# Kernel optimization log

Hardware: AMD Instinct MI355X
Metric: run time of the kernel (lower is better)

## Reference

```python
import jax, jax.numpy as jnp
import numpy as np

B, T, W, L, H = 32, 1024, 512, 12, 8
CH = W // H                      # per-head dim = 64
IN_CH = 3 + 6 + T                # x + params + class embedding channels = 1033
DFF = 4 * W
NEG = -100000.0
SCALE = 1.0 / np.sqrt(np.sqrt(CH))


def _layernorm(x, g, b, eps=1e-5):
    m = jnp.mean(x, axis=-1, keepdims=True)
    v = jnp.mean(jnp.square(x - m), axis=-1, keepdims=True)
    return (x - m) * jax.lax.rsqrt(v + eps) * g + b


def setup_inputs() -> dict:
    key = jax.random.key(0)
    ks = jax.random.split(key, 40)
    std = 0.25 * np.sqrt(1.0 / W)  # init_scale used inside Transformer

    def n(k, shape, s=std):
        return (jax.random.normal(k, shape, jnp.float32) * s).astype(jnp.float32)

    inp = {
        'x': jax.random.normal(ks[0], (B, 3, T), jnp.float32),
        'params': jax.random.normal(ks[1], (B, 6, T), jnp.float32),
        'mask': (jax.random.uniform(ks[2], (B, T)) > 0.2).astype(jnp.float32),
        'class_emb': jax.random.normal(ks[3], (T, T), jnp.float32),  # nn.Embedding(n_ctx, n_ctx)
        'w_in': n(ks[4], (IN_CH, W), 0.02), 'b_in': jnp.zeros((W,), jnp.float32),
        'ln_pre_g': jnp.ones((W,), jnp.float32), 'ln_pre_b': jnp.zeros((W,), jnp.float32),
        'qkv_w': n(ks[5], (L, W, 3 * W)), 'qkv_b': jnp.zeros((L, 3 * W), jnp.float32),
        'attn_pw': n(ks[6], (L, W, W)), 'attn_pb': jnp.zeros((L, W), jnp.float32),
        'ln1_g': jnp.ones((L, W), jnp.float32), 'ln1_b': jnp.zeros((L, W), jnp.float32),
        'fc_w': n(ks[7], (L, W, DFF)), 'fc_b': jnp.zeros((L, DFF), jnp.float32),
        'fcp_w': n(ks[8], (L, DFF, W)), 'fcp_b': jnp.zeros((L, W), jnp.float32),
        'ln2_g': jnp.ones((L, W), jnp.float32), 'ln2_b': jnp.zeros((L, W), jnp.float32),
        'ln_post_g': jnp.ones((W,), jnp.float32), 'ln_post_b': jnp.zeros((W,), jnp.float32),
        'w_out': n(ks[9], (W, W), 0.02), 'b_out': jnp.zeros((W,), jnp.float32),
        'agg_fc_w': n(ks[10], (W, DFF)), 'agg_fc_b': jnp.zeros((DFF,), jnp.float32),
        'agg_pw': n(ks[11], (DFF, W)), 'agg_pb': jnp.zeros((W,), jnp.float32),
    }
    return inp


def _block(h, p):
    qw, qb, pw, pb, l1g, l1b, fw, fb, gw, gb, l2g, l2b = p
    hn = _layernorm(h, l1g, l1b)
    qkv = (hn @ qw + qb).reshape(B, T, H, 3 * CH)
    q, k, v = jnp.split(qkv, 3, axis=-1)
    att = jnp.einsum('bthc,bshc->bhts', q * SCALE, k * SCALE)
    att = jax.nn.softmax(att.astype(jnp.float32), axis=-1)  # softmax in fp32
    o = jnp.einsum('bhts,bshc->bthc', att, v).reshape(B, T, W)
    h = h + o @ pw + pb
    hn2 = _layernorm(h, l2g, l2b)
    h = h + jax.nn.gelu(hn2 @ fw + fb, approximate=False) @ gw + gb
    return h, None


def reference(x, params, mask, class_emb, w_in, b_in, ln_pre_g, ln_pre_b,
              qkv_w, qkv_b, attn_pw, attn_pb, ln1_g, ln1_b, fc_w, fc_b,
              fcp_w, fcp_b, ln2_g, ln2_b, ln_post_g, ln_post_b, w_out, b_out,
              agg_fc_w, agg_fc_b, agg_pw, agg_pb):
    # concatenate params and class-embedding channels: [B, 1033, T]
    ce = jnp.broadcast_to(class_emb.T[None], (B, T, T))  # class_embed.transpose(1,2)
    xin = jnp.concatenate([x, params, ce], axis=1)
    h = jnp.einsum('bct,cw->btw', xin, w_in) + b_in      # input_proj on [B,T,1033]
    h = _layernorm(h, ln_pre_g, ln_pre_b)
    h, _ = jax.lax.scan(_block, h,
                        (qkv_w, qkv_b, attn_pw, attn_pb, ln1_g, ln1_b,
                         fc_w, fc_b, fcp_w, fcp_b, ln2_g, ln2_b))
    h = _layernorm(h, ln_post_g, ln_post_b)
    h = (h @ w_out + b_out).transpose(0, 2, 1)           # [B, 512, T]
    h = h * mask[:, None, :]
    pooled = jnp.max(h + (1.0 - mask[:, None, :]) * NEG, axis=2)  # [B, 512]
    z = jax.nn.gelu(pooled @ agg_fc_w + agg_fc_b, approximate=False) @ agg_pw + agg_pb
    return (z, h)
```

## Files before the change

kernel.cpp:

```cpp
#include <hip/hip_runtime.h>
#include <hip/hip_bf16.h>


typedef unsigned short u16;
typedef unsigned int u32;
typedef __attribute__((ext_vector_type(8))) short bf16x8;
typedef __attribute__((ext_vector_type(8))) unsigned short us8;
typedef __attribute__((ext_vector_type(4))) unsigned short us4;
typedef __attribute__((ext_vector_type(4))) float f32x4;

__device__ __forceinline__ float bf2f(u16 s) {
  union { u32 u; float f; } c; c.u = ((u32)s) << 16; return c.f;
}
__device__ __forceinline__ u16 f2bf(float f) {
  __hip_bfloat16 h = __float2bfloat16(f);
  union { __hip_bfloat16 h; u16 u; } c; c.h = h; return c.u;
}
__device__ __forceinline__ float gelu_f(float v) {
  return 0.5f * v * (1.0f + erff(v * 0.7071067811865475f));
}
__device__ __forceinline__ void gl2lds16(const u16* g, u16* l) {
  __builtin_amdgcn_global_load_lds((const __attribute__((address_space(1))) void*)g,
                                   (__attribute__((address_space(3))) void*)l, 16, 0, 0);
}
__device__ __forceinline__ f32x4 mfma16(bf16x8 a, bf16x8 b, f32x4 c) {
  return __builtin_amdgcn_mfma_f32_16x16x32_bf16(a, b, c, 0, 0, 0);
}
__device__ __forceinline__ int swz(int row) { return (row ^ (row >> 3)) & 7; }

template <int EPI>
__global__ __launch_bounds__(512)
void gemm_bt(const u16* __restrict__ A, const u16* __restrict__ Bt,
             const float* __restrict__ bias, float* __restrict__ Cf,
             u16* __restrict__ Cb, u16* __restrict__ Vt, int K, int lda, int ldb, int ldc)
{
  __shared__ __align__(16) u16 As[2][256 * 32];
  __shared__ __align__(16) u16 Bs[2][128 * 32];
  const int tid = threadIdx.x;
  const int lane = tid & 63, wid = tid >> 6;
  const int wm = wid & 3, wn = wid >> 2;
  const int nbx = gridDim.x;
  const int nwg = nbx * gridDim.y;
  int lin = blockIdx.y * nbx + blockIdx.x;
  lin = (lin & 7) * (nwg >> 3) + (lin >> 3);
  const long m0 = (long)(lin / nbx) * 256, n0 = (long)(lin % nbx) * 128;

  const int c0 = tid, c1 = tid + 512;
  const int kc0 = (c0 & 3) ^ (((c0 >> 2) >> 1) & 3);
  const int kc1 = (c1 & 3) ^ (((c1 >> 2) >> 1) & 3);
  const int kcb = (tid & 3) ^ (((tid >> 2) >> 1) & 3);
  const u16* aS0 = A + (m0 + (c0 >> 2)) * (long)lda + kc0 * 8;
  const u16* aS1 = A + (m0 + (c1 >> 2)) * (long)lda + kc1 * 8;
  const u16* bS0 = Bt + (n0 + (tid >> 2)) * (long)ldb + kcb * 8;

  f32x4 acc[4][4] = {};
  const int cl4 = lane & 15;
  const int gph = ((lane >> 4) ^ ((cl4 >> 1) & 3)) * 8;
  const int aro = (wm * 64 + cl4) * 32 + gph;
  const int bro = (wn * 64 + cl4) * 32 + gph;
  const int nt = K >> 5;

#define STAGE_AB(buf, k0_)                          \
  gl2lds16(aS0 + (k0_), As[buf] + c0 * 8);          \
  gl2lds16(aS1 + (k0_), As[buf] + c1 * 8);          \
  gl2lds16(bS0 + (k0_), Bs[buf] + tid * 8);

  STAGE_AB(0, 0);
  for (int t = 0; t < nt; ++t) {
    const int cur = t & 1;
    if (t < nt - 1) {
      STAGE_AB(cur ^ 1, (t + 1) * 32);
      asm volatile("s_waitcnt vmcnt(3)" ::: "memory");
    } else {
      asm volatile("s_waitcnt vmcnt(0)" ::: "memory");
    }
    __builtin_amdgcn_s_barrier();
    bf16x8 af[4], bfr[4];
#pragma unroll
    for (int i = 0; i < 4; ++i) af[i] = *(const bf16x8*)(As[cur] + aro + i * 16 * 32);
#pragma unroll
    for (int j = 0; j < 4; ++j) bfr[j] = *(const bf16x8*)(Bs[cur] + bro + j * 16 * 32);
    __builtin_amdgcn_s_setprio(1);
#pragma unroll
    for (int i = 0; i < 4; ++i)
#pragma unroll
      for (int j = 0; j < 4; ++j)
        acc[i][j] = mfma16(af[i], bfr[j], acc[i][j]);
    __builtin_amdgcn_s_setprio(0);
    __builtin_amdgcn_s_barrier();
  }
#undef STAGE_AB
  const int rg = (lane >> 4) * 4, cl = lane & 15;
#pragma unroll
  for (int i = 0; i < 4; ++i) {
#pragma unroll
    for (int j = 0; j < 4; ++j) {
      const long row = m0 + wm * 64 + i * 16 + rg;
      const long col = n0 + wn * 64 + j * 16 + cl;
      const float bv = bias ? bias[col] : 0.0f;
      if (EPI == 4) {
        const int hh = (int)col / 192, off = (int)col - hh * 192;
        if (off < 128) {
#pragma unroll
          for (int r = 0; r < 4; ++r)
            Cb[(row + r) * ldc + col] = f2bf(acc[i][j][r] + bv);
        } else {
          us4 pk;
#pragma unroll
          for (int r = 0; r < 4; ++r) pk[r] = f2bf(acc[i][j][r] + bv);
          const long bl = row >> 10, t0 = row & 1023;
          *(us4*)(Vt + (((bl * 8 + hh) * 64 + (off - 128)) << 10) + t0) = pk;
        }
      } else {
#pragma unroll
        for (int r = 0; r < 4; ++r) {
          float v = acc[i][j][r] + bv;
          long idx = (row + r) * ldc + col;
          if (EPI == 0) Cf[idx] = v;
          else if (EPI == 1) Cb[idx] = f2bf(v);
          else if (EPI == 2) Cf[idx] += v;
          else Cb[idx] = f2bf(gelu_f(v));
        }
      }
    }
  }
}

__global__ __launch_bounds__(512)
void attn_k(const u16* __restrict__ qkv, const u16* __restrict__ vt, u16* __restrict__ o)
{
  __shared__ __align__(16) u16 Qs[128 * 64];
  __shared__ __align__(16) u16 Ks[2][64 * 64];
  __shared__ __align__(16) u16 Vts[2][64 * 64];
  const int tid = threadIdx.x, lane = tid & 63, wid = tid >> 6;
  int lin = blockIdx.x;
  lin = (lin & 7) * 128 + (lin >> 3);
  const int qt = lin & 7, hh = (lin >> 3) & 7, b = lin >> 6;
  const long rowbase = (long)b * 1024;
  const long vbase = (((long)b * 8 + hh) * 64) * 1024;
  const int g = lane >> 4, cl = lane & 15;
  u16* Psw = Qs + wid * 1024;

#pragma unroll
  for (int it = 0; it < 2; ++it) {
    int c = tid + it * 512;
    int row = c >> 3, c8s = (c & 7) ^ swz(row);
    gl2lds16(qkv + (rowbase + qt * 128 + row) * 1536 + hh * 192 + c8s * 8, Qs + c * 8);
  }
#define STAGE_KV(buf, kt_)                                                            \
  {                                                                                   \
    int row = tid >> 3, c8s = (tid & 7) ^ swz(row);                                   \
    gl2lds16(qkv + (rowbase + (kt_) * 64 + row) * 1536 + hh * 192 + 64 + c8s * 8,     \
             Ks[buf] + tid * 8);                                                      \
    gl2lds16(vt + vbase + (long)row * 1024 + (kt_) * 64 + c8s * 8, Vts[buf] + tid * 8); \
  }
  STAGE_KV(0, 0);

  float m = -3.0e38f, l = 0.f;
  f32x4 oacc[4] = {};
  const int Rq = wid * 16 + cl, sq = swz(Rq) << 3;
  const int spw = swz(cl) << 3;
  bf16x8 aq[2];

  for (int kt = 0; kt < 16; ++kt) {
    const int cur = kt & 1;
    if (kt < 15) {
      STAGE_KV(cur ^ 1, kt + 1);
      asm volatile("s_waitcnt vmcnt(2)" ::: "memory");
    } else {
      asm volatile("s_waitcnt vmcnt(0)" ::: "memory");
    }
    __builtin_amdgcn_s_barrier();
    if (kt == 0) {
#pragma unroll
      for (int kb = 0; kb < 2; ++kb)
        aq[kb] = *(const bf16x8*)(Qs + Rq * 64 + ((kb * 32 + g * 8) ^ sq));
    }
    f32x4 s[4] = {};
    __builtin_amdgcn_s_setprio(1);
#pragma unroll
    for (int j = 0; j < 4; ++j) {
      const int Rk = j * 16 + cl, sk = swz(Rk) << 3;
#pragma unroll
      for (int kb = 0; kb < 2; ++kb) {
        bf16x8 bk = *(const bf16x8*)(Ks[cur] + Rk * 64 + ((kb * 32 + g * 8) ^ sk));
        s[j] = mfma16(bk, aq[kb], s[j]);
      }
    }
    __builtin_amdgcn_s_setprio(0);
    float mx = s[0][0];
#pragma unroll
    for (int j = 0; j < 4; ++j)
#pragma unroll
      for (int r = 0; r < 4; ++r) mx = fmaxf(mx, s[j][r]);
    mx *= 0.125f;
    mx = fmaxf(mx, __shfl_xor(mx, 16, 64));
    mx = fmaxf(mx, __shfl_xor(mx, 32, 64));
    if (!__all(mx <= m + 8.f)) {
      const float mnew = fmaxf(m, mx);
      const float al = __expf(m - mnew);
      m = mnew;
      l *= al;
      float alr[4];
#pragma unroll
      for (int r = 0; r < 4; ++r) alr[r] = __shfl(al, (lane & 48) | (g * 4 + r), 64);
#pragma unroll
      for (int cb = 0; cb < 4; ++cb) {
        f32x4 t = oacc[cb];
        t[0] *= alr[0]; t[1] *= alr[1]; t[2] *= alr[2]; t[3] *= alr[3];
        oacc[cb] = t;
      }
    }
    float p[4][4], ts = 0.f;
#pragma unroll
    for (int j = 0; j < 4; ++j)
#pragma unroll
      for (int r = 0; r < 4; ++r) {
        p[j][r] = __expf(s[j][r] * 0.125f - m);
        ts += p[j][r];
      }
    ts += __shfl_xor(ts, 16, 64);
    ts += __shfl_xor(ts, 32, 64);
    l += ts;
#pragma unroll
    for (int j = 0; j < 4; ++j) {
      us4 pk;
      pk[0] = f2bf(p[j][0]); pk[1] = f2bf(p[j][1]);
      pk[2] = f2bf(p[j][2]); pk[3] = f2bf(p[j][3]);
      *(us4*)(&Psw[cl * 64 + ((j * 16 + g * 4) ^ spw)]) = pk;
    }
    asm volatile("s_waitcnt lgkmcnt(0)" ::: "memory");
    bf16x8 pa[2];
#pragma unroll
    for (int kb = 0; kb < 2; ++kb)
      pa[kb] = *(const bf16x8*)(&Psw[cl * 64 + ((kb * 32 + g * 8) ^ spw)]);
    __builtin_amdgcn_s_setprio(1);
#pragma unroll
    for (int kb = 0; kb < 2; ++kb)
#pragma unroll
      for (int cb = 0; cb < 4; ++cb) {
        const int ch = cb * 16 + cl;
        bf16x8 vb = *(const bf16x8*)(Vts[cur] + ch * 64 + ((kb * 32 + g * 8) ^ (swz(ch) << 3)));
        oacc[cb] = mfma16(pa[kb], vb, oacc[cb]);
      }
    __builtin_amdgcn_s_setprio(0);
    __builtin_amdgcn_s_barrier();
  }
#undef STAGE_KV
  float lr[4];
#pragma unroll
  for (int r = 0; r < 4; ++r) lr[r] = __shfl(l, (lane & 48) | (g * 4 + r), 64);
#pragma unroll
  for (int cb = 0; cb < 4; ++cb)
#pragma unroll
    for (int r = 0; r < 4; ++r) {
      long row = rowbase + qt * 128 + wid * 16 + g * 4 + r;
      o[row * 512 + hh * 64 + cb * 16 + cl] = f2bf(oacc[cb][r] / lr[r]);
    }
}

template <int MODE>
__global__ __launch_bounds__(256)
void ln_k(const float* __restrict__ in_, const float* __restrict__ gg,
          const float* __restrict__ bb, void* __restrict__ out_)
{
  const long row = (long)blockIdx.x * 4 + (threadIdx.x >> 6);
  const int lane = threadIdx.x & 63;
  float x[8];
  const float* p = in_ + row * 512 + lane * 8;
  *(float4*)(x) = *(const float4*)(p);
  *(float4*)(x + 4) = *(const float4*)(p + 4);
  float s = 0.f;
#pragma unroll
  for (int j = 0; j < 8; ++j) s += x[j];
#pragma unroll
  for (int off = 1; off < 64; off <<= 1) s += __shfl_xor(s, off, 64);
  const float mean = s * (1.0f / 512.0f);
  float vs = 0.f;
#pragma unroll
  for (int j = 0; j < 8; ++j) { float d = x[j] - mean; vs += d * d; }
#pragma unroll
  for (int off = 1; off < 64; off <<= 1) vs += __shfl_xor(vs, off, 64);
  const float rstd = rsqrtf(vs * (1.0f / 512.0f) + 1e-5f);
  if (MODE == 0) {
    float y[8];
#pragma unroll
    for (int j = 0; j < 8; ++j)
      y[j] = (x[j] - mean) * rstd * gg[lane * 8 + j] + bb[lane * 8 + j];
    float* q = (float*)out_ + row * 512 + lane * 8;
    *(float4*)(q) = *(const float4*)(y);
    *(float4*)(q + 4) = *(const float4*)(y + 4);
  } else {
    us8 ov;
#pragma unroll
    for (int j = 0; j < 8; ++j)
      ov[j] = f2bf((x[j] - mean) * rstd * gg[lane * 8 + j] + bb[lane * 8 + j]);
    *(us8*)((u16*)out_ + row * 512 + lane * 8) = ov;
  }
}

__global__ __launch_bounds__(256)
void embed_k(const float* __restrict__ x, const float* __restrict__ par,
             const float* __restrict__ E, const float* __restrict__ w_in,
             const float* __restrict__ b_in, float* __restrict__ h)
{
  const long bt = blockIdx.x;
  const int b = (int)(bt >> 10), t = (int)(bt & 1023);
  float xs[9];
#pragma unroll
  for (int c = 0; c < 3; ++c) xs[c] = x[((long)b * 3 + c) * 1024 + t];
#pragma unroll
  for (int c = 0; c < 6; ++c) xs[3 + c] = par[((long)b * 6 + c) * 1024 + t];
  for (int w = threadIdx.x; w < 512; w += 256) {
    float a = E[(long)t * 512 + w] + b_in[w];
#pragma unroll
    for (int c = 0; c < 9; ++c) a += xs[c] * w_in[c * 512 + w];
    h[bt * 512 + w] = a;
  }
}

__global__ __launch_bounds__(256)
void tr_k(const float* __restrict__ in, u16* __restrict__ out, int R, int C)
{
  __shared__ u16 tile[32][33];
  const int r0 = blockIdx.y * 32, c0 = blockIdx.x * 32;
  const int tx = threadIdx.x & 31, ty = threadIdx.x >> 5;
  for (int rr = ty; rr < 32; rr += 8) tile[rr][tx] = f2bf(in[(long)(r0 + rr) * C + c0 + tx]);
  __syncthreads();
  for (int rr = ty; rr < 32; rr += 8) out[(long)(c0 + rr) * R + r0 + tx] = tile[tx][rr];
}

__global__ __launch_bounds__(256)
void cast_k(const float* __restrict__ in, u16* __restrict__ out, long n)
{
  long i = ((long)blockIdx.x * 256 + threadIdx.x) * 4;
  if (i + 3 < n) {
    float4 v = *(const float4*)(in + i);
    out[i] = f2bf(v.x); out[i + 1] = f2bf(v.y); out[i + 2] = f2bf(v.z); out[i + 3] = f2bf(v.w);
  }
}

__global__ __launch_bounds__(256)
void pool1_k(const float* __restrict__ hm, const float* __restrict__ mask, float* __restrict__ part)
{
  const int c = blockIdx.x, b = blockIdx.y;
  const int t0 = c * 128;
  const int w0 = threadIdx.x, w1 = threadIdx.x + 256;
  float m0 = -3.0e38f, m1 = -3.0e38f;
  for (int t = 0; t < 128; ++t) {
    const float mv = mask[b * 1024 + t0 + t];
    const float neg = (1.0f - mv) * (-100000.0f);
    const float* row = hm + ((long)b * 1024 + t0 + t) * 512;
    m0 = fmaxf(m0, row[w0] * mv + neg);
    m1 = fmaxf(m1, row[w1] * mv + neg);
  }
  part[((long)b * 8 + c) * 512 + w0] = m0;
  part[((long)b * 8 + c) * 512 + w1] = m1;
}
__global__ __launch_bounds__(256)
void pool2_k(const float* __restrict__ part, float* __restrict__ pooled)
{
  const int b = blockIdx.y;
  const int w = blockIdx.x * 256 + threadIdx.x;
  float m = -3.0e38f;
#pragma unroll
  for (int c = 0; c < 8; ++c) m = fmaxf(m, part[((long)b * 8 + c) * 512 + w]);
  pooled[b * 512 + w] = m;
}

__global__ __launch_bounds__(256)
void tout_k(const float* __restrict__ hm, const float* __restrict__ mask, float* __restrict__ outh)
{
  __shared__ float tile[64][65];
  const int t0 = blockIdx.x * 64, w0 = blockIdx.y * 64, b = blockIdx.z;
  const int tx = threadIdx.x & 63, ty = threadIdx.x >> 6;
  for (int i = ty; i < 64; i += 4)
    tile[i][tx] = hm[((long)b * 1024 + t0 + i) * 512 + w0 + tx];
  __syncthreads();
  const float mv = mask[b * 1024 + t0 + tx];
  for (int i = ty; i < 64; i += 4)
    outh[((long)b * 512 + w0 + i) * 1024 + t0 + tx] = tile[tx][i] * mv;
}

__global__ __launch_bounds__(256)
void agg1p_k(const float* __restrict__ pooled, const float* __restrict__ wf,
             float* __restrict__ part)
{
  const int b = blockIdx.z, kc = blockIdx.y;
  const int n = blockIdx.x * 256 + threadIdx.x;
  float acc = 0.f;
  const int k0 = kc * 64;
#pragma unroll 8
  for (int k = 0; k < 64; ++k) acc += pooled[b * 512 + k0 + k] * wf[(long)(k0 + k) * 2048 + n];
  part[((long)b * 8 + kc) * 2048 + n] = acc;
}
__global__ __launch_bounds__(256)
void agg1c_k(const float* __restrict__ part, const float* __restrict__ bf_,
             float* __restrict__ z1)
{
  const int b = blockIdx.y;
  const int n = blockIdx.x * 256 + threadIdx.x;
  float acc = 0.f;
#pragma unroll
  for (int c = 0; c < 8; ++c) acc += part[((long)b * 8 + c) * 2048 + n];
  z1[(long)b * 2048 + n] = gelu_f(acc + bf_[n]);
}
__global__ __launch_bounds__(256)
void agg2p_k(const float* __restrict__ z1, const float* __restrict__ wp,
             float* __restrict__ part)
{
  const int b = blockIdx.z, kc = blockIdx.y;
  const int n = blockIdx.x * 256 + threadIdx.x;
  float acc = 0.f;
  const int k0 = kc * 256;
#pragma unroll 8
  for (int k = 0; k < 256; ++k) acc += z1[(long)b * 2048 + k0 + k] * wp[(long)(k0 + k) * 512 + n];
  part[((long)b * 8 + kc) * 512 + n] = acc;
}
__global__ __launch_bounds__(256)
void agg2c_k(const float* __restrict__ part, const float* __restrict__ bp,
             float* __restrict__ zo)
{
  const int b = blockIdx.y;
  const int n = blockIdx.x * 256 + threadIdx.x;
  float acc = 0.f;
#pragma unroll
  for (int c = 0; c < 8; ++c) acc += part[((long)b * 8 + c) * 512 + n];
  zo[b * 512 + n] = acc + bp[n];
}

extern "C" void kernel_launch(void* const* d_in, const int* in_sizes, int n_in,
                              void* d_out, int out_size, void* d_ws, size_t ws_size,
                              hipStream_t stream)
{
  (void)in_sizes; (void)n_in; (void)out_size; (void)ws_size;
  const float* x        = (const float*)d_in[0];
  const float* params   = (const float*)d_in[1];
  const float* mask     = (const float*)d_in[2];
  const float* class_emb= (const float*)d_in[3];
  const float* w_in     = (const float*)d_in[4];
  const float* b_in     = (const float*)d_in[5];
  const float* ln_pre_g = (const float*)d_in[6];
  const float* ln_pre_b = (const float*)d_in[7];
  const float* qkv_w    = (const float*)d_in[8];
  const float* qkv_b    = (const float*)d_in[9];
  const float* attn_pw  = (const float*)d_in[10];
  const float* attn_pb  = (const float*)d_in[11];
  const float* ln1_g    = (const float*)d_in[12];
  const float* ln1_b    = (const float*)d_in[13];
  const float* fc_w     = (const float*)d_in[14];
  const float* fc_b     = (const float*)d_in[15];
  const float* fcp_w    = (const float*)d_in[16];
  const float* fcp_b    = (const float*)d_in[17];
  const float* ln2_g    = (const float*)d_in[18];
  const float* ln2_b    = (const float*)d_in[19];
  const float* ln_post_g= (const float*)d_in[20];
  const float* ln_post_b= (const float*)d_in[21];
  const float* w_out    = (const float*)d_in[22];
  const float* b_out    = (const float*)d_in[23];
  const float* agg_fc_w = (const float*)d_in[24];
  const float* agg_fc_b = (const float*)d_in[25];
  const float* agg_pw   = (const float*)d_in[26];
  const float* agg_pb   = (const float*)d_in[27];

  float* out_f = (float*)d_out;
  float* out_h = out_f + 16384;
  u16* sc = (u16*)out_h;

  char* ws = (char*)d_ws;
  float* hf = (float*)ws;       ws += (size_t)32768 * 512 * 4;
  u16* hn = (u16*)ws;           ws += (size_t)32768 * 512 * 2;
  float* E = (float*)ws;        ws += (size_t)1024 * 512 * 4;
  u16* ce_b = (u16*)ws;         ws += (size_t)1024 * 1024 * 2;
  u16* wt_qkv = (u16*)ws;       ws += (size_t)1536 * 512 * 2;
  u16* wt_pw  = (u16*)ws;       ws += (size_t)512 * 512 * 2;
  u16* wt_fc  = (u16*)ws;       ws += (size_t)2048 * 512 * 2;
  u16* wt_fcp = (u16*)ws;       ws += (size_t)512 * 2048 * 2;
  u16* w_in_t = (u16*)ws;       ws += (size_t)512 * 1024 * 2;
  u16* w_out_t= (u16*)ws;       ws += (size_t)512 * 512 * 2;
  float* pooled = (float*)ws;   ws += (size_t)32 * 512 * 4;
  float* z1     = (float*)ws;   ws += (size_t)32 * 2048 * 4;
  float* part   = (float*)ws;   ws += (size_t)32 * 8 * 512 * 4;
  float* apart1 = (float*)ws;   ws += (size_t)32 * 8 * 2048 * 4;
  float* apart2 = (float*)ws;   ws += (size_t)32 * 8 * 512 * 4;
  u16* vt       = (u16*)ws;     ws += (size_t)16 * 8 * 64 * 1024 * 2;

  cast_k<<<1024, 256, 0, stream>>>(class_emb, ce_b, 1024 * 1024);
  tr_k<<<dim3(16, 32), 256, 0, stream>>>(w_in + 9 * 512, w_in_t, 1024, 512);
  tr_k<<<dim3(16, 16), 256, 0, stream>>>(w_out, w_out_t, 512, 512);
  gemm_bt<0><<<dim3(4, 4), 512, 0, stream>>>(ce_b, w_in_t, nullptr, E, nullptr, nullptr,
                                             1024, 1024, 1024, 512);
  embed_k<<<32768, 256, 0, stream>>>(x, params, E, w_in, b_in, hf);
  ln_k<0><<<8192, 256, 0, stream>>>(hf, ln_pre_g, ln_pre_b, hf);

  for (int l = 0; l < 12; ++l) {
    tr_k<<<dim3(48, 16), 256, 0, stream>>>(qkv_w + (size_t)l * 512 * 1536, wt_qkv, 512, 1536);
    tr_k<<<dim3(16, 16), 256, 0, stream>>>(attn_pw + (size_t)l * 512 * 512, wt_pw, 512, 512);
    tr_k<<<dim3(64, 16), 256, 0, stream>>>(fc_w + (size_t)l * 512 * 2048, wt_fc, 512, 2048);
    tr_k<<<dim3(16, 64), 256, 0, stream>>>(fcp_w + (size_t)l * 2048 * 512, wt_fcp, 2048, 512);

    ln_k<1><<<8192, 256, 0, stream>>>(hf, ln1_g + l * 512, ln1_b + l * 512, hn);
    for (int half = 0; half < 2; ++half) {
      const size_t ro = (size_t)half * 16384;
      gemm_bt<4><<<dim3(12, 64), 512, 0, stream>>>(hn + ro * 512, wt_qkv, qkv_b + l * 1536,
                                                   nullptr, sc, vt, 512, 512, 512, 1536);
      attn_k<<<1024, 512, 0, stream>>>(sc, vt, hn + ro * 512);
    }
    gemm_bt<2><<<dim3(4, 128), 512, 0, stream>>>(hn, wt_pw, attn_pb + l * 512,
                                                 hf, nullptr, nullptr, 512, 512, 512, 512);
    ln_k<1><<<8192, 256, 0, stream>>>(hf, ln2_g + l * 512, ln2_b + l * 512, hn);
    for (int half = 0; half < 2; ++half) {
      const size_t ro = (size_t)half * 16384;
      gemm_bt<3><<<dim3(16, 64), 512, 0, stream>>>(hn + ro * 512, wt_fc, fc_b + l * 2048,
                                                   nullptr, sc, nullptr, 512, 512, 512, 2048);
      gemm_bt<2><<<dim3(4, 64), 512, 0, stream>>>(sc, wt_fcp, fcp_b + l * 512,
                                                  hf + ro * 512, nullptr, nullptr, 2048, 2048, 2048, 512);
    }
  }

  ln_k<1><<<8192, 256, 0, stream>>>(hf, ln_post_g, ln_post_b, hn);
  gemm_bt<0><<<dim3(4, 128), 512, 0, stream>>>(hn, w_out_t, b_out, hf, nullptr, nullptr,
                                               512, 512, 512, 512);
  pool1_k<<<dim3(8, 32), 256, 0, stream>>>(hf, mask, part);
  pool2_k<<<dim3(2, 32), 256, 0, stream>>>(part, pooled);
  agg1p_k<<<dim3(8, 8, 32), 256, 0, stream>>>(pooled, agg_fc_w, apart1);
  agg1c_k<<<dim3(8, 32), 256, 0, stream>>>(apart1, agg_fc_b, z1);
  agg2p_k<<<dim3(2, 8, 32), 256, 0, stream>>>(z1, agg_pw, apart2);
  agg2c_k<<<dim3(2, 32), 256, 0, stream>>>(apart2, agg_pb, out_f);
  tout_k<<<dim3(16, 8, 32), 256, 0, stream>>>(hf, mask, out_h);
}
```

Baseline: 6.590 ms.

## Add 256x256-tile GEMM for FC layer and merge per-layer weight transposes

Adds a new GEMM kernel with 1024-thread blocks and 256x256 output tiles, double-buffered via direct global-to-LDS loads, and uses it for the FC (GELU) projection in place of the smaller-tile kernel. The larger tile raises operand reuse per LDS load and lowers global traffic, at the cost of fewer workgroups and higher register and LDS use per block. It also merges the four per-layer weight-transpose launches into one kernel that dispatches on block index, which cuts launch overhead.

```diff
diff --git a/kernel.cpp b/kernel.cpp
--- a/kernel.cpp
+++ b/kernel.cpp
@@ -121,6 +121,84 @@
           else if (EPI == 2) Cf[idx] += v;
           else Cb[idx] = f2bf(gelu_f(v));
         }
+      }
+    }
+  }
+}
+
+template <int EPI>
+__global__ __launch_bounds__(1024)
+void gemm_bt2(const u16* __restrict__ A, const u16* __restrict__ Bt,
+              const float* __restrict__ bias, float* __restrict__ Cf,
+              u16* __restrict__ Cb, int K, int lda, int ldb, int ldc)
+{
+  __shared__ __align__(16) u16 As[2][256 * 32];
+  __shared__ __align__(16) u16 Bs[2][256 * 32];
+  const int tid = threadIdx.x;
+  const int lane = tid & 63, wid = tid >> 6;
+  const int wm = wid & 3, wn = wid >> 2;
+  const int nbx = gridDim.x;
+  const int nwg = nbx * gridDim.y;
+  int lin = blockIdx.y * nbx + blockIdx.x;
+  lin = (lin & 7) * (nwg >> 3) + (lin >> 3);
+  const long m0 = (long)(lin / nbx) * 256, n0 = (long)(lin % nbx) * 256;
+
+  const int kcA = (tid & 3) ^ (((tid >> 2) >> 1) & 3);
+  const u16* aS0 = A + (m0 + (tid >> 2)) * (long)lda + kcA * 8;
+  const u16* bS0 = Bt + (n0 + (tid >> 2)) * (long)ldb + kcA * 8;
+
+  f32x4 acc[4][4] = {};
+  const int cl4 = lane & 15;
+  const int gph = ((lane >> 4) ^ ((cl4 >> 1) & 3)) * 8;
+  const int aro = (wm * 64 + cl4) * 32 + gph;
+  const int bro = (wn * 64 + cl4) * 32 + gph;
+  const int nt = K >> 5;
+
+#define STAGE_AB2(buf, k0_)                         \
+  gl2lds16(aS0 + (k0_), As[buf] + tid * 8);         \
+  gl2lds16(bS0 + (k0_), Bs[buf] + tid * 8);
+
+  STAGE_AB2(0, 0);
+  for (int t = 0; t < nt; ++t) {
+    const int cur = t & 1;
+    if (t < nt - 1) {
+      STAGE_AB2(cur ^ 1, (t + 1) * 32);
+      asm volatile("s_waitcnt vmcnt(2)" ::: "memory");
+    } else {
+      asm volatile("s_waitcnt vmcnt(0)" ::: "memory");
+    }
+    __builtin_amdgcn_s_barrier();
+    bf16x8 af[4], bfr[4];
+#pragma unroll
+    for (int i = 0; i < 4; ++i) af[i] = *(const bf16x8*)(As[cur] + aro + i * 16 * 32);
+#pragma unroll
+    for (int j = 0; j < 4; ++j) bfr[j] = *(const bf16x8*)(Bs[cur] + bro + j * 16 * 32);
+    __builtin_amdgcn_s_setprio(1);
+#pragma unroll
+    for (int i = 0; i < 4; ++i)
+#pragma unroll
+      for (int j = 0; j < 4; ++j)
+        acc[i][j] = mfma16(af[i], bfr[j], acc[i][j]);
+    __builtin_amdgcn_s_setprio(0);
+    __builtin_amdgcn_s_barrier();
+  }
+#undef STAGE_AB2
+  const int rg = (lane >> 4) * 4, cl = lane & 15;
+#pragma unroll
+  for (int i = 0; i < 4; ++i) {
+#pragma unroll
+    for (int j = 0; j < 4; ++j) {
+      const long row = m0 + wm * 64 + i * 16 + rg;
+      const long col = n0 + wn * 64 + j * 16 + cl;
+      const float bv = bias ? bias[col] : 0.0f;
+#pragma unroll
+      for (int r = 0; r < 4; ++r) {
+        float v = acc[i][j][r] + bv;
+        long idx = (row + r) * ldc + col;
+        if (EPI == 0) Cf[idx] = v;
+        else if (EPI == 1) Cb[idx] = f2bf(v);
+        else if (EPI == 2) Cf[idx] += v;
+        else Cb[idx] = f2bf(gelu_f(v));
       }
     }
   }
@@ -328,6 +406,26 @@
   for (int rr = ty; rr < 32; rr += 8) tile[rr][tx] = f2bf(in[(long)(r0 + rr) * C + c0 + tx]);
   __syncthreads();
   for (int rr = ty; rr < 32; rr += 8) out[(long)(c0 + rr) * R + r0 + tx] = tile[tx][rr];
+}
+
+__global__ __launch_bounds__(256)
+void trL_k(const float* __restrict__ qkv_w, const float* __restrict__ pw,
+           const float* __restrict__ fcw, const float* __restrict__ fcpw,
+           u16* __restrict__ o_qkv, u16* __restrict__ o_pw,
+           u16* __restrict__ o_fc, u16* __restrict__ o_fcp)
+{
+  __shared__ u16 tile[32][33];
+  int bid = blockIdx.x;
+  const float* src; u16* dst; int R, C, bx, by;
+  if (bid < 768)       { src = qkv_w; dst = o_qkv; R = 512;  C = 1536; bx = bid % 48; by = bid / 48; }
+  else if (bid < 1024) { bid -= 768;  src = pw;   dst = o_pw;  R = 512;  C = 512;  bx = bid % 16; by = bid / 16; }
+  else if (bid < 2048) { bid -= 1024; src = fcw;  dst = o_fc;  R = 512;  C = 2048; bx = bid % 64; by = bid / 64; }
+  else                 { bid -= 2048; src = fcpw; dst = o_fcp; R = 2048; C = 512;  bx = bid % 16; by = bid / 16; }
+  const int r0 = by * 32, c0 = bx * 32;
+  const int tx = threadIdx.x & 31, ty = threadIdx.x >> 5;
+  for (int rr = ty; rr < 32; rr += 8) tile[rr][tx] = f2bf(src[(long)(r0 + rr) * C + c0 + tx]);
+  __syncthreads();
+  for (int rr = ty; rr < 32; rr += 8) dst[(long)(c0 + rr) * R + r0 + tx] = tile[tx][rr];
 }
 
 __global__ __launch_bounds__(256)
@@ -494,10 +592,11 @@
   ln_k<0><<<8192, 256, 0, stream>>>(hf, ln_pre_g, ln_pre_b, hf);
 
   for (int l = 0; l < 12; ++l) {
-    tr_k<<<dim3(48, 16), 256, 0, stream>>>(qkv_w + (size_t)l * 512 * 1536, wt_qkv, 512, 1536);
-    tr_k<<<dim3(16, 16), 256, 0, stream>>>(attn_pw + (size_t)l * 512 * 512, wt_pw, 512, 512);
-    tr_k<<<dim3(64, 16), 256, 0, stream>>>(fc_w + (size_t)l * 512 * 2048, wt_fc, 512, 2048);
-    tr_k<<<dim3(16, 64), 256, 0, stream>>>(fcp_w + (size_t)l * 2048 * 512, wt_fcp, 2048, 512);
+    trL_k<<<3072, 256, 0, stream>>>(qkv_w + (size_t)l * 512 * 1536,
+                                    attn_pw + (size_t)l * 512 * 512,
+                                    fc_w + (size_t)l * 512 * 2048,
+                                    fcp_w + (size_t)l * 2048 * 512,
+                                    wt_qkv, wt_pw, wt_fc, wt_fcp);
 
     ln_k<1><<<8192, 256, 0, stream>>>(hf, ln1_g + l * 512, ln1_b + l * 512, hn);
     for (int half = 0; half < 2; ++half) {
@@ -511,8 +610,8 @@
     ln_k<1><<<8192, 256, 0, stream>>>(hf, ln2_g + l * 512, ln2_b + l * 512, hn);
     for (int half = 0; half < 2; ++half) {
       const size_t ro = (size_t)half * 16384;
-      gemm_bt<3><<<dim3(16, 64), 512, 0, stream>>>(hn + ro * 512, wt_fc, fc_b + l * 2048,
-                                                   nullptr, sc, nullptr, 512, 512, 512, 2048);
+      gemm_bt2<3><<<dim3(8, 64), 1024, 0, stream>>>(hn + ro * 512, wt_fc, fc_b + l * 2048,
+                                                    nullptr, sc, 512, 512, 512, 2048);
       gemm_bt<2><<<dim3(4, 64), 512, 0, stream>>>(sc, wt_fcp, fcp_b + l * 512,
                                                   hf + ro * 512, nullptr, nullptr, 2048, 2048, 2048, 512);
     }
```

Measured after the change: 6.518 ms. No clear change (-1.1%).
